# Performance work log

Hardware: AMD Instinct MI355X
Metric: run time of the kernel (lower is better)

Reference implementation:

```python
import jax, jax.numpy as jnp
import numpy as np

N_NODES = 50000
N_EDGES = 400000
F_IN = 128
HEADS = 4
C1 = 64
C2 = 16
OUT_DIM = 2
N_GRAPHS = 64
NEG_SLOPE = 0.2


def setup_inputs() -> dict:
    key = jax.random.key(0)
    ks = jax.random.split(key, 16)
    s = 0.05
    x = jax.random.normal(ks[0], (N_NODES, F_IN), jnp.float32)
    edge_index = jax.random.randint(ks[1], (27, N_EDGES), 0, N_NODES, dtype=jnp.int32)
    batch = jnp.sort(jax.random.randint(ks[2], (N_NODES,), 0, N_GRAPHS, dtype=jnp.int32))
    return {
        "x": x,
        "edge_index": edge_index,
        "batch": batch,
        "W1": jax.random.normal(ks[3], (F_IN, HEADS * C1), jnp.float32) * s,
        "a_src1": jax.random.normal(ks[4], (HEADS, C1), jnp.float32) * s,
        "a_dst1": jax.random.normal(ks[5], (HEADS, C1), jnp.float32) * s,
        "b1": jnp.zeros((HEADS * C1,), jnp.float32),
        "W2": jax.random.normal(ks[6], (HEADS * C1, HEADS * C2), jnp.float32) * s,
        "a_src2": jax.random.normal(ks[7], (HEADS, C2), jnp.float32) * s,
        "a_dst2": jax.random.normal(ks[8], (HEADS, C2), jnp.float32) * s,
        "b2": jnp.zeros((HEADS * C2,), jnp.float32),
        "Wfc": jax.random.normal(ks[9], (HEADS * C2, OUT_DIM), jnp.float32) * s,
        "bfc": jnp.zeros((OUT_DIM,), jnp.float32),
    }


def gat_layer(x, src, dst, W, a_src, a_dst, b, out_ch):
    """PyG GATConv (concat=True, add_self_loops=True, negative_slope=0.2)."""
    n = x.shape[0]
    h = (x @ W).reshape(n, HEADS, out_ch)            # [N,H,C]
    # add self-loops (PyG default)
    loop = jnp.arange(n, dtype=src.dtype)
    src = jnp.concatenate([src, loop])
    dst = jnp.concatenate([dst, loop])
    alpha_s = jnp.einsum("nhc,hc->nh", h, a_src)      # [N,H]
    alpha_d = jnp.einsum("nhc,hc->nh", h, a_dst)
    e = jax.nn.leaky_relu(alpha_s[src] + alpha_d[dst], NEG_SLOPE)  # [E,H]
    # segment softmax over incoming edges per destination node
    m = jax.ops.segment_max(e, dst, num_segments=n)
    exp_e = jnp.exp(e - m[dst])
    denom = jax.ops.segment_sum(exp_e, dst, num_segments=n)
    alpha = exp_e / (denom[dst] + 1e-16)              # [E,H]
    out = jax.ops.segment_sum(alpha[:, :, None] * h[src], dst, num_segments=n)
    return out.reshape(n, HEADS * out_ch) + b


def reference(x, edge_index, batch, W1, a_src1, a_dst1, b1, W2, a_src2, a_dst2, b2, Wfc, bfc):
    # conv1 uses rows [17, 26] as (src, dst)
    h = gat_layer(x, edge_index[17], edge_index[26], W1, a_src1, a_dst1, b1, C1)
    h = jax.nn.relu(h)
    # conv2 uses rows [15,16,17,24,25,26]; message passing reads rows 0,1 -> (15,16)
    h = gat_layer(h, edge_index[15], edge_index[16], W2, a_src2, a_dst2, b2, C2)
    h = jax.nn.relu(h)
    # global mean pool over graphs
    sums = jax.ops.segment_sum(h, batch, num_segments=N_GRAPHS)
    cnts = jax.ops.segment_sum(jnp.ones((h.shape[0], 1), h.dtype), batch, num_segments=N_GRAPHS)
    pooled = sums / jnp.maximum(cnts, 1.0)
    return pooled @ Wfc + bfc
```

## Files before the change

kernel.cpp:

```cpp
#include <hip/hip_runtime.h>
#include <math.h>

#define HEADS 4
#define NEG_SLOPE 0.2f
#define CAP 32

static constexpr size_t OFF_H1B  = 0;
static constexpr size_t OFF_H2B  = 0;
static constexpr size_t OFF_OUT2 = 6400000;
static constexpr size_t OFF_XHI  = 25600000;
static constexpr size_t OFF_XLO  = 38400000;
static constexpr size_t OFF_O1HI = 25600000;
static constexpr size_t OFF_W1TH = 76800000;
static constexpr size_t OFF_W1TL = 76865536;
static constexpr size_t OFF_W2TH = 76931072;
static constexpr size_t OFF_W2TL = 76963840;
static constexpr size_t OFF_AS   = 77000000;
static constexpr size_t OFF_AD   = 77800000;
static constexpr size_t OFF_CNT  = 78600064;
static constexpr size_t OFF_CSR  = 79000128;

typedef __attribute__((ext_vector_type(8))) short short8;
typedef __attribute__((ext_vector_type(4))) float f32x4;

__device__ __forceinline__ float4 f4add(float4 a, float4 b) {
    return make_float4(a.x + b.x, a.y + b.y, a.z + b.z, a.w + b.w);
}
__device__ __forceinline__ float lrelu(float x) { return x > 0.f ? x : NEG_SLOPE * x; }
__device__ __forceinline__ float4 f4lrelu(float4 a) {
    return make_float4(lrelu(a.x), lrelu(a.y), lrelu(a.z), lrelu(a.w));
}
__device__ __forceinline__ float4 f4exp(float4 a) {
    return make_float4(__expf(a.x), __expf(a.y), __expf(a.z), __expf(a.w));
}
__device__ __forceinline__ float pickh(float4 v, int head) {
    float r = v.x;
    r = head == 1 ? v.y : r;
    r = head == 2 ? v.z : r;
    r = head == 3 ? v.w : r;
    return r;
}
__device__ __forceinline__ unsigned short bfr(float x) {
    union { float f; unsigned u; } c; c.f = x;
    unsigned r = c.u + 0x7FFFu + ((c.u >> 16) & 1u);
    return (unsigned short)(r >> 16);
}
__device__ __forceinline__ float bf2f(unsigned short h) {
    union { unsigned u; float f; } c; c.u = ((unsigned)h) << 16;
    return c.f;
}
__device__ __forceinline__ float2 bfpair(unsigned u) {
    union { unsigned a; float f; } lo, hi;
    lo.a = u << 16;
    hi.a = u & 0xffff0000u;
    return make_float2(lo.f, hi.f);
}

__global__ void prep_kernel(const float* __restrict__ x, unsigned short* __restrict__ xhi,
                            unsigned short* __restrict__ xlo, int n4,
                            const float* __restrict__ W1, unsigned short* __restrict__ w1th,
                            unsigned short* __restrict__ w1tl,
                            const float* __restrict__ W2, unsigned short* __restrict__ w2th,
                            unsigned short* __restrict__ w2tl,
                            int* __restrict__ cnt, int n2)
{
    const int b = blockIdx.x, t = threadIdx.x;
    if (b < 1024) {
        for (int i = b * 256 + t; i < n4; i += 1024 * 256) {
            float4 v = ((const float4*)x)[i];
            unsigned short h0 = bfr(v.x), h1 = bfr(v.y), h2 = bfr(v.z), h3 = bfr(v.w);
            unsigned short l0 = bfr(v.x - bf2f(h0)), l1 = bfr(v.y - bf2f(h1));
            unsigned short l2 = bfr(v.z - bf2f(h2)), l3 = bfr(v.w - bf2f(h3));
            ((uint2*)xhi)[i] = make_uint2((unsigned)h0 | ((unsigned)h1 << 16),
                                          (unsigned)h2 | ((unsigned)h3 << 16));
            ((uint2*)xlo)[i] = make_uint2((unsigned)l0 | ((unsigned)l1 << 16),
                                          (unsigned)l2 | ((unsigned)l3 << 16));
        }
    } else if (b < 1024 + 128) {
        int idx = (b - 1024) * 256 + t;
        const int K = 128, Nc = 256;
        int k = idx / Nc, n = idx - k * Nc;
        float v = W1[idx];
        unsigned short h = bfr(v);
        w1th[(size_t)n * K + k] = h;
        w1tl[(size_t)n * K + k] = bfr(v - bf2f(h));
    } else if (b < 1024 + 128 + 64) {
        int idx = (b - 1152) * 256 + t;
        const int K = 256, Nc = 64;
        int k = idx / Nc, n = idx - k * Nc;
        float v = W2[idx];
        unsigned short h = bfr(v);
        w2th[(size_t)n * K + k] = h;
        w2tl[(size_t)n * K + k] = bfr(v - bf2f(h));
    } else {
        int idx = (b - 1216) * 256 + t;
        if (idx < (n2 >> 2)) ((int4*)cnt)[idx] = make_int4(0, 0, 0, 0);
    }
}

__global__ void bucket_kernel(const int* __restrict__ src1, const int* __restrict__ dst1,
                              const int* __restrict__ src2, const int* __restrict__ dst2,
                              int* __restrict__ cnt, int* __restrict__ csr, int N, int E)
{
    const int part  = blockIdx.x & 7;
    const int chunk = blockIdx.x >> 3;
    const int base  = chunk * 2048 + threadIdx.x;
#pragma unroll
    for (int k = 0; k < 8; ++k) {
        int e = base + k * 256;
        if (e < E) {
            int d = dst1[e];
            if ((d & 7) == part) {
                int p = atomicAdd(&cnt[d], 1);
                if (p < CAP) csr[(size_t)d * CAP + p] = src1[e];
            }
        } else if (e < 2 * E) {
            int d = dst2[e - E];
            if ((d & 7) == part) {
                int p = atomicAdd(&cnt[N + d], 1);
                if (p < CAP) csr[((size_t)N + d) * CAP + p] = src2[e - E];
            }
        }
    }
}

template<int BM, int BN, int KDIM, int WR, int WC, int CPH, bool ALO>
__global__ __launch_bounds__(256, 2)
void mfma_gemm_gat(const unsigned short* __restrict__ Ahi, const unsigned short* __restrict__ Alo,
                   const unsigned short* __restrict__ BThi, const unsigned short* __restrict__ BTlo,
                   unsigned short* __restrict__ Cb,
                   const float* __restrict__ avec_s, const float* __restrict__ avec_d,
                   float* __restrict__ alpha_s, float* __restrict__ alpha_d,
                   int M, int N)
{
    constexpr int BK    = 32;
    constexpr int WROWS = BM / WR;
    constexpr int WCOLS = BN / WC;
    constexpr int FR    = WROWS / 16;
    constexpr int FC    = WCOLS / 16;
    constexpr int AP    = (BM * (BK / 8)) / 256;
    constexpr int BP    = (BN * (BK / 8)) / 256;
    static_assert(AP >= 1 && BP >= 1, "tile too small");

    __shared__ short As_hi[BM * BK], As_lo[ALO ? BM * BK : 64];
    __shared__ short Bs_hi[BN * BK], Bs_lo[BN * BK];

    const int tid  = threadIdx.x;
    const int w    = tid >> 6, lane = tid & 63;
    const int wr   = w / WC, wc = w % WC;
    const int lrow = lane & 15, lk = lane >> 4;
    const int m0   = blockIdx.x * BM, n0 = blockIdx.y * BN;

    f32x4 acc[FR][FC];
#pragma unroll
    for (int i = 0; i < FR; ++i)
#pragma unroll
        for (int j = 0; j < FC; ++j) acc[i][j] = (f32x4){0.f, 0.f, 0.f, 0.f};

    short8 rAh[AP], rAl[AP], rBh[BP], rBl[BP];

    auto LOAD = [&](int kb) {
#pragma unroll
        for (int p = 0; p < AP; ++p) {
            int id = p * 256 + tid;
            int r = id >> 2, c = id & 3;
            int row = m0 + r; row = row < M ? row : M - 1;
            size_t off = (size_t)row * KDIM + kb + c * 8;
            rAh[p] = *(const short8*)(Ahi + off);
            if constexpr (ALO) rAl[p] = *(const short8*)(Alo + off);
        }
#pragma unroll
        for (int p = 0; p < BP; ++p) {
            int id = p * 256 + tid;
            int r = id >> 2, c = id & 3;
            size_t off = (size_t)(n0 + r) * KDIM + kb + c * 8;
            rBh[p] = *(const short8*)(BThi + off);
            rBl[p] = *(const short8*)(BTlo + off);
        }
    };
    auto STORE = [&]() {
#pragma unroll
        for (int p = 0; p < AP; ++p) {
            int id = p * 256 + tid;
            int r = id >> 2, c = id & 3;
            *(short8*)(&As_hi[r * BK + c * 8]) = rAh[p];
            if constexpr (ALO) *(short8*)(&As_lo[r * BK + c * 8]) = rAl[p];
        }
#pragma unroll
        for (int p = 0; p < BP; ++p) {
            int id = p * 256 + tid;
            int r = id >> 2, c = id & 3;
            *(short8*)(&Bs_hi[r * BK + c * 8]) = rBh[p];
            *(short8*)(&Bs_lo[r * BK + c * 8]) = rBl[p];
        }
    };

    constexpr int NT = KDIM / BK;
    LOAD(0);
    for (int t = 0; t < NT; ++t) {
        STORE();
        __syncthreads();
        if (t + 1 < NT) LOAD((t + 1) * BK);

        short8 afh[FR], afl[FR], bfh[FC], bfl[FC];
#pragma unroll
        for (int fr = 0; fr < FR; ++fr) {
            int r = wr * WROWS + fr * 16 + lrow;
            afh[fr] = *(const short8*)(&As_hi[r * BK + lk * 8]);
            if constexpr (ALO) afl[fr] = *(const short8*)(&As_lo[r * BK + lk * 8]);
        }
#pragma unroll
        for (int fc = 0; fc < FC; ++fc) {
            int r = wc * WCOLS + fc * 16 + lrow;
            bfh[fc] = *(const short8*)(&Bs_hi[r * BK + lk * 8]);
            bfl[fc] = *(const short8*)(&Bs_lo[r * BK + lk * 8]);
        }
#pragma unroll
        for (int fr = 0; fr < FR; ++fr)
#pragma unroll
            for (int fc = 0; fc < FC; ++fc) {
                acc[fr][fc] = __builtin_amdgcn_mfma_f32_16x16x32_bf16(afh[fr], bfh[fc], acc[fr][fc], 0, 0, 0);
                acc[fr][fc] = __builtin_amdgcn_mfma_f32_16x16x32_bf16(afh[fr], bfl[fc], acc[fr][fc], 0, 0, 0);
                if constexpr (ALO)
                    acc[fr][fc] = __builtin_amdgcn_mfma_f32_16x16x32_bf16(afl[fr], bfh[fc], acc[fr][fc], 0, 0, 0);
            }
        __syncthreads();
    }

#pragma unroll
    for (int fr = 0; fr < FR; ++fr) {
        const int rbase = m0 + wr * WROWS + fr * 16 + lk * 4;
        float ps[4] = {0.f, 0.f, 0.f, 0.f}, pd[4] = {0.f, 0.f, 0.f, 0.f};
#pragma unroll
        for (int fc = 0; fc < FC; ++fc) {
            const int gc   = n0 + wc * WCOLS + fc * 16 + lrow;
            const int head = gc / CPH, ci = gc % CPH;
            const float asv = avec_s[head * CPH + ci];
            const float adv = avec_d[head * CPH + ci];
#pragma unroll
            for (int rg = 0; rg < 4; ++rg) {
                int row = rbase + rg;
                float v = acc[fr][fc][rg];
                unsigned short uh = bfr(v);
                unsigned up = (unsigned)__shfl_xor((int)(unsigned)uh, 1);
                if (!(lrow & 1) && row < M)
                    *(unsigned*)(Cb + (size_t)row * N + gc) = (unsigned)uh | (up << 16);
                ps[rg] += v * asv;
                pd[rg] += v * adv;
            }
            if constexpr (CPH == 16) {
#pragma unroll
                for (int rg = 0; rg < 4; ++rg) {
                    float s = ps[rg], d = pd[rg];
#pragma unroll
                    for (int m = 1; m <= 8; m <<= 1) {
                        s += __shfl_xor(s, m);
                        d += __shfl_xor(d, m);
                    }
                    if (lrow == 0 && rbase + rg < M) {
                        alpha_s[(size_t)(rbase + rg) * HEADS + head] = s;
                        alpha_d[(size_t)(rbase + rg) * HEADS + head] = d;
                    }
                    ps[rg] = 0.f; pd[rg] = 0.f;
                }
            }
        }
        if constexpr (CPH != 16) {
            const int head = (n0 + wc * WCOLS) / CPH;
#pragma unroll
            for (int rg = 0; rg < 4; ++rg) {
                float s = ps[rg], d = pd[rg];
#pragma unroll
                for (int m = 1; m <= 8; m <<= 1) {
                    s += __shfl_xor(s, m);
                    d += __shfl_xor(d, m);
                }
                if (lrow == 0 && rbase + rg < M) {
                    alpha_s[(size_t)(rbase + rg) * HEADS + head] = s;
                    alpha_d[(size_t)(rbase + rg) * HEADS + head] = d;
                }
            }
        }
    }
}

template<int CH, int S, bool OUTF32>
__global__ __launch_bounds__(256)
void gat_agg(const unsigned short* __restrict__ hb, const float* __restrict__ alpha_s,
             const float* __restrict__ alpha_d, const int* __restrict__ cnt,
             const int* __restrict__ csr, const float* __restrict__ bias,
             float* __restrict__ out, unsigned short* __restrict__ out_hi, int n)
{
    constexpr int CPL = CH / S;
    constexpr int NSG = 256 / S;
    static_assert(CPL == 8, "lane owns one uint4");
    __shared__ float wls[NSG][S * 5];
    const int tid    = threadIdx.x;
    const int sub    = tid / S;
    const int i      = tid % S;
    const int lane64 = tid & 63;
    const int base   = lane64 & ~(S - 1);
    const int node   = blockIdx.x * NSG + sub;
    if (node >= n) return;
    const int head = (i * CPL) / (CH / 4);
    const int deg = min(cnt[node], CAP);
    const size_t ebase = (size_t)node * CAP;

    const float4 asn = *(const float4*)(alpha_s + (size_t)node * 4);
    const float4 adn = *(const float4*)(alpha_d + (size_t)node * 4);
    float4 den = f4exp(f4lrelu(f4add(asn, adn)));
    const float wse = pickh(den, head);

    float acc[8];
    {
        uint4 hv = *(const uint4*)(hb + (size_t)node * CH + i * 8);
        float2 q0 = bfpair(hv.x), q1 = bfpair(hv.y), q2 = bfpair(hv.z), q3 = bfpair(hv.w);
        acc[0] = wse * q0.x; acc[1] = wse * q0.y; acc[2] = wse * q1.x; acc[3] = wse * q1.y;
        acc[4] = wse * q2.x; acc[5] = wse * q2.y; acc[6] = wse * q3.x; acc[7] = wse * q3.y;
    }

    for (int ch = 0; ch < deg; ch += S) {
        const int cntc = min(S, deg - ch);
        float4 w4 = make_float4(0.f, 0.f, 0.f, 0.f);
        int sl = 0;
        if (i < cntc) {
            sl = csr[ebase + ch + i];
            float4 al = *(const float4*)(alpha_s + (size_t)sl * 4);
            w4 = f4exp(f4lrelu(f4add(al, adn)));
        }
        float4 t = w4;
#pragma unroll
        for (int d = S / 2; d >= 1; d >>= 1) {
            t.x += __shfl_xor(t.x, d);
            t.y += __shfl_xor(t.y, d);
            t.z += __shfl_xor(t.z, d);
            t.w += __shfl_xor(t.w, d);
        }
        den = f4add(den, t);
        wls[sub][i * 5 + 0] = w4.x;
        wls[sub][i * 5 + 1] = w4.y;
        wls[sub][i * 5 + 2] = w4.z;
        wls[sub][i * 5 + 3] = w4.w;

        const int padded = (cntc + 7) & ~7;
        for (int j = 0; j < padded; j += 8) {
            int   sk[8];
            float wk[8];
#pragma unroll
            for (int k = 0; k < 8; ++k) {
                sk[k] = __shfl(sl, base + ((j + k) < S ? (j + k) : 0));
                wk[k] = wls[sub][(j + k) * 5 + head];
            }
            uint4 v[8];
#pragma unroll
            for (int k = 0; k < 8; ++k)
                v[k] = *(const uint4*)(hb + (size_t)sk[k] * CH + i * 8);
#pragma unroll
            for (int k = 0; k < 8; ++k) {
                float2 q0 = bfpair(v[k].x), q1 = bfpair(v[k].y);
                float2 q2 = bfpair(v[k].z), q3 = bfpair(v[k].w);
                acc[0] += wk[k] * q0.x; acc[1] += wk[k] * q0.y;
                acc[2] += wk[k] * q1.x; acc[3] += wk[k] * q1.y;
                acc[4] += wk[k] * q2.x; acc[5] += wk[k] * q2.y;
                acc[6] += wk[k] * q3.x; acc[7] += wk[k] * q3.y;
            }
        }
    }

    const float invd = 1.0f / (pickh(den, head) + 1e-16f);
    const int c0 = i * CPL;
    float o[8];
#pragma unroll
    for (int k = 0; k < 8; ++k)
        o[k] = fmaxf(acc[k] * invd + bias[c0 + k], 0.f);
    if constexpr (OUTF32) {
        *(float4*)(out + (size_t)node * CH + c0)     = make_float4(o[0], o[1], o[2], o[3]);
        *(float4*)(out + (size_t)node * CH + c0 + 4) = make_float4(o[4], o[5], o[6], o[7]);
    } else {
        unsigned short oh[8];
#pragma unroll
        for (int k = 0; k < 8; ++k) oh[k] = bfr(o[k]);
        uint4 ph;
        ph.x = (unsigned)oh[0] | ((unsigned)oh[1] << 16);
        ph.y = (unsigned)oh[2] | ((unsigned)oh[3] << 16);
        ph.z = (unsigned)oh[4] | ((unsigned)oh[5] << 16);
        ph.w = (unsigned)oh[6] | ((unsigned)oh[7] << 16);
        *(uint4*)(out_hi + (size_t)node * CH + c0) = ph;
    }
}

__global__ __launch_bounds__(256)
void pool_fc_kernel(const float* __restrict__ feat, const int* __restrict__ batch,
                    const float* __restrict__ Wfc, const float* __restrict__ bfc,
                    float* __restrict__ out, int n)
{
    __shared__ float4 part[16][16];
    __shared__ float pooled[64];
    __shared__ int sb[2];
    const int g = blockIdx.x;
    const int t = threadIdx.x;
    if (t < 2) {
        int target = g + t;
        int lo = 0, hi = n;
        while (lo < hi) {
            int mid = (lo + hi) >> 1;
            if (batch[mid] < target) lo = mid + 1; else hi = mid;
        }
        sb[t] = lo;
    }
    __syncthreads();
    const int s0 = sb[0], s1 = sb[1];
    const int q = t & 15, ns = t >> 4;
    float4 acc = make_float4(0.f, 0.f, 0.f, 0.f);
    for (int i = s0 + ns; i < s1; i += 16)
        acc = f4add(acc, *(const float4*)(feat + (size_t)i * 64 + q * 4));
    part[ns][q] = acc;
    __syncthreads();
    if (t < 16) {
        float4 s = part[0][t];
#pragma unroll
        for (int k = 1; k < 16; ++k) s = f4add(s, part[k][t]);
        float inv = 1.0f / fmaxf((float)(s1 - s0), 1.0f);
        pooled[t * 4 + 0] = s.x * inv;
        pooled[t * 4 + 1] = s.y * inv;
        pooled[t * 4 + 2] = s.z * inv;
        pooled[t * 4 + 3] = s.w * inv;
    }
    __syncthreads();
    if (t < 2) {
        float a = bfc[t];
        for (int c = 0; c < 64; ++c) a += pooled[c] * Wfc[c * 2 + t];
        out[g * 2 + t] = a;
    }
}

extern "C" void kernel_launch(void* const* d_in, const int* in_sizes, int n_in,
                              void* d_out, int out_size, void* d_ws, size_t ws_size,
                              hipStream_t stream)
{
    const float* x    = (const float*)d_in[0];
    const int*   ei   = (const int*)d_in[1];
    const int*   batch= (const int*)d_in[2];
    const float* W1   = (const float*)d_in[3];
    const float* as1  = (const float*)d_in[4];
    const float* ad1  = (const float*)d_in[5];
    const float* b1   = (const float*)d_in[6];
    const float* W2   = (const float*)d_in[7];
    const float* as2  = (const float*)d_in[8];
    const float* ad2  = (const float*)d_in[9];
    const float* b2   = (const float*)d_in[10];
    const float* Wfc  = (const float*)d_in[11];
    const float* bfc  = (const float*)d_in[12];
    float* out = (float*)d_out;

    const int N = in_sizes[2];
    const int E = in_sizes[1] / 27;
    const int F = in_sizes[0] / N;

    char* ws = (char*)d_ws;
    unsigned short* h1b   = (unsigned short*)(ws + OFF_H1B);
    unsigned short* h2b   = (unsigned short*)(ws + OFF_H2B);
    float*          out2  = (float*)(ws + OFF_OUT2);
    unsigned short* xhi   = (unsigned short*)(ws + OFF_XHI);
    unsigned short* xlo   = (unsigned short*)(ws + OFF_XLO);
    unsigned short* o1hi  = (unsigned short*)(ws + OFF_O1HI);
    unsigned short* w1th  = (unsigned short*)(ws + OFF_W1TH);
    unsigned short* w1tl  = (unsigned short*)(ws + OFF_W1TL);
    unsigned short* w2th  = (unsigned short*)(ws + OFF_W2TH);
    unsigned short* w2tl  = (unsigned short*)(ws + OFF_W2TL);
    float* al_s  = (float*)(ws + OFF_AS);
    float* al_d  = (float*)(ws + OFF_AD);
    int*   cnt   = (int*)(ws + OFF_CNT);
    int*   csr   = (int*)(ws + OFF_CSR);

    const int NCH = (2 * E + 2047) / 2048;
    const int ZB  = ((2 * N / 4) + 255) / 256;

    prep_kernel<<<1216 + ZB, 256, 0, stream>>>(x, xhi, xlo, N * F / 4,
                                               W1, w1th, w1tl, W2, w2th, w2tl,
                                               cnt, 2 * N);

    bucket_kernel<<<NCH * 8, 256, 0, stream>>>(ei + 17 * (size_t)E, ei + 26 * (size_t)E,
                                               ei + 15 * (size_t)E, ei + 16 * (size_t)E,
                                               cnt, csr, N, E);

    {
        dim3 g((N + 63) / 64, 2);
        mfma_gemm_gat<64, 128, 128, 2, 2, 64, true><<<g, 256, 0, stream>>>(
            xhi, xlo, w1th, w1tl, h1b, as1, ad1, al_s, al_d, N, HEADS * 64);
    }
    gat_agg<256, 32, false><<<(N + 7) / 8, 256, 0, stream>>>(h1b, al_s, al_d, cnt, csr, b1,
                                                             nullptr, o1hi, N);

    {
        dim3 g((N + 63) / 64, 1);
        mfma_gemm_gat<64, 64, 256, 2, 2, 16, false><<<g, 256, 0, stream>>>(
            o1hi, nullptr, w2th, w2tl, h2b, as2, ad2, al_s, al_d, N, HEADS * 16);
    }
    gat_agg<64, 8, true><<<(N + 31) / 32, 256, 0, stream>>>(h2b, al_s, al_d, cnt + N,
                                                            csr + (size_t)N * CAP, b2,
                                                            out2, nullptr, N);

    pool_fc_kernel<<<64, 256, 0, stream>>>(out2, batch, Wfc, bfc, out, N);
}
```

Baseline: 168.3 us.

## Merge edge bucketing into layer-1 GEMM launch as extra blocks

```diff
diff --git a/kernel.cpp b/kernel.cpp
--- a/kernel.cpp
+++ b/kernel.cpp
@@ -98,27 +98,172 @@
     }
 }
 
-__global__ void bucket_kernel(const int* __restrict__ src1, const int* __restrict__ dst1,
-                              const int* __restrict__ src2, const int* __restrict__ dst2,
-                              int* __restrict__ cnt, int* __restrict__ csr, int N, int E)
+__global__ __launch_bounds__(256, 2)
+void gemm1_bucket_kernel(const unsigned short* __restrict__ Ahi, const unsigned short* __restrict__ Alo,
+                         const unsigned short* __restrict__ BThi, const unsigned short* __restrict__ BTlo,
+                         unsigned short* __restrict__ Cb,
+                         const float* __restrict__ avec_s, const float* __restrict__ avec_d,
+                         float* __restrict__ alpha_s, float* __restrict__ alpha_d,
+                         int M, int N, int GX,
+                         const int* __restrict__ src1, const int* __restrict__ dst1,
+                         const int* __restrict__ src2, const int* __restrict__ dst2,
+                         int* __restrict__ cnt, int* __restrict__ csr, int NN, int E)
 {
-    const int part  = blockIdx.x & 7;
-    const int chunk = blockIdx.x >> 3;
-    const int base  = chunk * 2048 + threadIdx.x;
-#pragma unroll
-    for (int k = 0; k < 8; ++k) {
-        int e = base + k * 256;
-        if (e < E) {
-            int d = dst1[e];
-            if ((d & 7) == part) {
-                int p = atomicAdd(&cnt[d], 1);
-                if (p < CAP) csr[(size_t)d * CAP + p] = src1[e];
-            }
-        } else if (e < 2 * E) {
-            int d = dst2[e - E];
-            if ((d & 7) == part) {
-                int p = atomicAdd(&cnt[N + d], 1);
-                if (p < CAP) csr[((size_t)N + d) * CAP + p] = src2[e - E];
+    constexpr int BM = 64, BN = 128, KDIM = 128, WC = 2, CPH = 64;
+    constexpr int BK    = 32;
+    constexpr int WROWS = 32;
+    constexpr int WCOLS = 64;
+    constexpr int FR    = 2;
+    constexpr int FC    = 4;
+    constexpr int AP    = 1;
+    constexpr int BP    = 2;
+
+    __shared__ short As_hi[BM * BK], As_lo[BM * BK];
+    __shared__ short Bs_hi[BN * BK], Bs_lo[BN * BK];
+
+    const int GEMM_CNT = GX * 2;
+
+    if ((int)blockIdx.x >= GEMM_CNT) {
+        const int b     = blockIdx.x - GEMM_CNT;
+        const int part  = b & 7;
+        const int chunk = b >> 3;
+        const int base  = chunk * 2048 + threadIdx.x;
+#pragma unroll
+        for (int k = 0; k < 8; ++k) {
+            int e = base + k * 256;
+            if (e < E) {
+                int d = dst1[e];
+                if ((d & 7) == part) {
+                    int p = atomicAdd(&cnt[d], 1);
+                    if (p < CAP) csr[(size_t)d * CAP + p] = src1[e];
+                }
+            } else if (e < 2 * E) {
+                int d = dst2[e - E];
+                if ((d & 7) == part) {
+                    int p = atomicAdd(&cnt[NN + d], 1);
+                    if (p < CAP) csr[((size_t)NN + d) * CAP + p] = src2[e - E];
+                }
+            }
+        }
+        return;
+    }
+
+    const int bx = blockIdx.x % GX, by = blockIdx.x / GX;
+    const int tid  = threadIdx.x;
+    const int w    = tid >> 6, lane = tid & 63;
+    const int wr   = w / WC, wc = w % WC;
+    const int lrow = lane & 15, lk = lane >> 4;
+    const int m0   = bx * BM, n0 = by * BN;
+
+    f32x4 acc[FR][FC];
+#pragma unroll
+    for (int i = 0; i < FR; ++i)
+#pragma unroll
+        for (int j = 0; j < FC; ++j) acc[i][j] = (f32x4){0.f, 0.f, 0.f, 0.f};
+
+    short8 rAh[AP], rAl[AP], rBh[BP], rBl[BP];
+
+    auto LOAD = [&](int kb) {
+#pragma unroll
+        for (int p = 0; p < AP; ++p) {
+            int id = p * 256 + tid;
+            int r = id >> 2, c = id & 3;
+            int row = m0 + r; row = row < M ? row : M - 1;
+            size_t off = (size_t)row * KDIM + kb + c * 8;
+            rAh[p] = *(const short8*)(Ahi + off);
+            rAl[p] = *(const short8*)(Alo + off);
+        }
+#pragma unroll
+        for (int p = 0; p < BP; ++p) {
+            int id = p * 256 + tid;
+            int r = id >> 2, c = id & 3;
+            size_t off = (size_t)(n0 + r) * KDIM + kb + c * 8;
+            rBh[p] = *(const short8*)(BThi + off);
+            rBl[p] = *(const short8*)(BTlo + off);
+        }
+    };
+    auto STORE = [&]() {
+#pragma unroll
+        for (int p = 0; p < AP; ++p) {
+            int id = p * 256 + tid;
+            int r = id >> 2, c = id & 3;
+            *(short8*)(&As_hi[r * BK + c * 8]) = rAh[p];
+            *(short8*)(&As_lo[r * BK + c * 8]) = rAl[p];
+        }
+#pragma unroll
+        for (int p = 0; p < BP; ++p) {
+            int id = p * 256 + tid;
+            int r = id >> 2, c = id & 3;
+            *(short8*)(&Bs_hi[r * BK + c * 8]) = rBh[p];
+            *(short8*)(&Bs_lo[r * BK + c * 8]) = rBl[p];
+        }
+    };
+
+    constexpr int NT = KDIM / BK;
+    LOAD(0);
+    for (int t = 0; t < NT; ++t) {
+        STORE();
+        __syncthreads();
+        if (t + 1 < NT) LOAD((t + 1) * BK);
+
+        short8 afh[FR], afl[FR], bfh[FC], bfl[FC];
+#pragma unroll
+        for (int fr = 0; fr < FR; ++fr) {
+            int r = wr * WROWS + fr * 16 + lrow;
+            afh[fr] = *(const short8*)(&As_hi[r * BK + lk * 8]);
+            afl[fr] = *(const short8*)(&As_lo[r * BK + lk * 8]);
+        }
+#pragma unroll
+        for (int fc = 0; fc < FC; ++fc) {
+            int r = wc * WCOLS + fc * 16 + lrow;
+            bfh[fc] = *(const short8*)(&Bs_hi[r * BK + lk * 8]);
+            bfl[fc] = *(const short8*)(&Bs_lo[r * BK + lk * 8]);
+        }
+#pragma unroll
+        for (int fr = 0; fr < FR; ++fr)
+#pragma unroll
+            for (int fc = 0; fc < FC; ++fc) {
+                acc[fr][fc] = __builtin_amdgcn_mfma_f32_16x16x32_bf16(afh[fr], bfh[fc], acc[fr][fc], 0, 0, 0);
+                acc[fr][fc] = __builtin_amdgcn_mfma_f32_16x16x32_bf16(afh[fr], bfl[fc], acc[fr][fc], 0, 0, 0);
+                acc[fr][fc] = __builtin_amdgcn_mfma_f32_16x16x32_bf16(afl[fr], bfh[fc], acc[fr][fc], 0, 0, 0);
+            }
+        __syncthreads();
+    }
+
+#pragma unroll
+    for (int fr = 0; fr < FR; ++fr) {
+        const int rbase = m0 + wr * WROWS + fr * 16 + lk * 4;
+        float ps[4] = {0.f, 0.f, 0.f, 0.f}, pd[4] = {0.f, 0.f, 0.f, 0.f};
+#pragma unroll
+        for (int fc = 0; fc < FC; ++fc) {
+            const int gc   = n0 + wc * WCOLS + fc * 16 + lrow;
+            const int head = gc / CPH, ci = gc % CPH;
+            const float asv = avec_s[head * CPH + ci];
+            const float adv = avec_d[head * CPH + ci];
+#pragma unroll
+            for (int rg = 0; rg < 4; ++rg) {
+                int row = rbase + rg;
+                float v = acc[fr][fc][rg];
+                unsigned short uh = bfr(v);
+                unsigned up = (unsigned)__shfl_xor((int)(unsigned)uh, 1);
+                if (!(lrow & 1) && row < M)
+                    *(unsigned*)(Cb + (size_t)row * N + gc) = (unsigned)uh | (up << 16);
+                ps[rg] += v * asv;
+                pd[rg] += v * adv;
+            }
+        }
+        const int head = (n0 + wc * WCOLS) / CPH;
+#pragma unroll
+        for (int rg = 0; rg < 4; ++rg) {
+            float s = ps[rg], d = pd[rg];
+#pragma unroll
+            for (int m = 1; m <= 8; m <<= 1) {
+                s += __shfl_xor(s, m);
+                d += __shfl_xor(d, m);
+            }
+            if (lrow == 0 && rbase + rg < M) {
+                alpha_s[(size_t)(rbase + rg) * HEADS + head] = s;
+                alpha_d[(size_t)(rbase + rg) * HEADS + head] = d;
             }
         }
     }
@@ -475,20 +620,18 @@
 
     const int NCH = (2 * E + 2047) / 2048;
     const int ZB  = ((2 * N / 4) + 255) / 256;
+    const int GX  = (N + 63) / 64;
 
     prep_kernel<<<1216 + ZB, 256, 0, stream>>>(x, xhi, xlo, N * F / 4,
                                                W1, w1th, w1tl, W2, w2th, w2tl,
                                                cnt, 2 * N);
 
-    bucket_kernel<<<NCH * 8, 256, 0, stream>>>(ei + 17 * (size_t)E, ei + 26 * (size_t)E,
-                                               ei + 15 * (size_t)E, ei + 16 * (size_t)E,
-                                               cnt, csr, N, E);
-
-    {
-        dim3 g((N + 63) / 64, 2);
-        mfma_gemm_gat<64, 128, 128, 2, 2, 64, true><<<g, 256, 0, stream>>>(
-            xhi, xlo, w1th, w1tl, h1b, as1, ad1, al_s, al_d, N, HEADS * 64);
-    }
+    gemm1_bucket_kernel<<<GX * 2 + NCH * 8, 256, 0, stream>>>(
+        xhi, xlo, w1th, w1tl, h1b, as1, ad1, al_s, al_d, N, HEADS * 64, GX,
+        ei + 17 * (size_t)E, ei + 26 * (size_t)E,
+        ei + 15 * (size_t)E, ei + 16 * (size_t)E,
+        cnt, csr, N, E);
+
     gat_agg<256, 32, false><<<(N + 7) / 8, 256, 0, stream>>>(h1b, al_s, al_d, cnt, csr, b1,
                                                              nullptr, o1hi, N);
 
```

New measurement: 159.8 us. 5.1% less time.
